# Kernel tuning notes

Measured on AMD Instinct MI355X. Metric: run time of the kernel, lower is better.

## Reference

```python
import jax, jax.numpy as jnp
import numpy as np

EPS = 1e-8  # torch F.cosine_similarity default eps


def setup_inputs() -> dict:
    key = jax.random.key(0)
    k1, k2, k3, k4 = jax.random.split(key, 4)
    B, S, D_in, D_e, E = 4, 128, 768, 256, 100000
    return {
        "x": jax.random.normal(k1, (B, S, D_in), dtype=jnp.float32),
        "W": jax.random.normal(k2, (D_e, D_in), dtype=jnp.float32) * 0.02,
        "b": jax.random.normal(k3, (D_e,), dtype=jnp.float32) * 0.02,
        "entity_embedding": jax.random.normal(k4, (E, D_e), dtype=jnp.float32),
    }


def reference(x, W, b, entity_embedding):
    # Linear projection + tanh: [B,S,D_e]
    q = jnp.tanh(jnp.einsum('bsi,ei->bse', x, W) + b)
    # Cosine similarity = L2-normalize both sides, then GEMM (fused; avoids
    # the [B,S,E,D] broadcast intermediate of the original).
    qn = q / jnp.maximum(jnp.linalg.norm(q, axis=-1, keepdims=True), EPS)
    en = entity_embedding / jnp.maximum(
        jnp.linalg.norm(entity_embedding, axis=-1, keepdims=True), EPS)
    return jnp.einsum('bsd,ed->bse', qn, en)  # [B,S,E]
```

## Files before the change

kernel.cpp:

```cpp
#include <hip/hip_runtime.h>
#include <hip/hip_bf16.h>

#define D_IN  768
#define D_E   256
#define M_TOT 512
#define E_TOT 100000

typedef __attribute__((ext_vector_type(4))) float f32x4;
typedef __attribute__((ext_vector_type(8))) short bf16x8;

__device__ __forceinline__ unsigned short bf16bits(float f) {
    union { __hip_bfloat16 h; unsigned short u; } c;
    c.h = __float2bfloat16(f);
    return c.u;
}

__device__ __forceinline__ void gload_lds16(const void* g, void* l) {
    __builtin_amdgcn_global_load_lds(
        (const __attribute__((address_space(1))) void*)g,
        (__attribute__((address_space(3))) void*)l, 16, 0, 0);
}

#define PROJ_BLOCKS 64
#define PREP_BLOCKS 1563
#define PP_GRID (PROJ_BLOCKS + PREP_BLOCKS)
#define PTM 8
#define PBK 64
#define PROUNDS (D_IN / PBK)

__global__ __launch_bounds__(512) void fused_pp(
    const float* __restrict__ x, const float* __restrict__ W,
    const float* __restrict__ b, const float* __restrict__ en,
    unsigned short* __restrict__ qb, unsigned short* __restrict__ eb)
{
    __shared__ float ws[D_E * (PBK + 1)];
    __shared__ float xs[PTM][PBK];
    __shared__ float red[PTM][4];
    __shared__ float qiv[PTM];

    const int t   = threadIdx.x;
    const int bid = blockIdx.x;

    if (bid >= PROJ_BLOCKS) {
        const int lane = t & 63;
        const int gw   = (bid - PROJ_BLOCKS) * 8 + (t >> 6);
        #pragma unroll 2
        for (int i = 0; i < 8; ++i) {
            const int row = gw * 8 + i;
            if (row >= E_TOT) break;
            const float4 v = *reinterpret_cast<const float4*>(
                en + (size_t)row * D_E + lane * 4);
            float s = v.x*v.x + v.y*v.y + v.z*v.z + v.w*v.w;
            #pragma unroll
            for (int off = 1; off < 64; off <<= 1) s += __shfl_xor(s, off, 64);
            const float sc = 1.0f / fmaxf(sqrtf(s), 1e-8f);
            union { unsigned short u[4]; uint2 d; } o;
            o.u[0] = bf16bits(v.x * sc); o.u[1] = bf16bits(v.y * sc);
            o.u[2] = bf16bits(v.z * sc); o.u[3] = bf16bits(v.w * sc);
            *reinterpret_cast<uint2*>(eb + (size_t)row * D_E + lane * 4) = o.d;
        }
        return;
    }

    const int m0   = bid * PTM;
    const int e    = t & 255;
    const int half = t >> 8;
    const int c4   = t & 15;
    const int rr   = t >> 4;

    float4 wreg[8];
    float  xreg = 0.f;
    float  acc[4] = {0.f, 0.f, 0.f, 0.f};

    #pragma unroll
    for (int i = 0; i < 8; ++i)
        wreg[i] = *reinterpret_cast<const float4*>(
            &W[(size_t)(i * 32 + rr) * D_IN + c4 * 4]);
    xreg = x[(size_t)(m0 + (t >> 6)) * D_IN + (t & 63)];

    for (int rd = 0; rd < PROUNDS; ++rd) {
        #pragma unroll
        for (int i = 0; i < 8; ++i) {
            float* dst = &ws[(i * 32 + rr) * (PBK + 1) + c4 * 4];
            dst[0] = wreg[i].x; dst[1] = wreg[i].y;
            dst[2] = wreg[i].z; dst[3] = wreg[i].w;
        }
        xs[t >> 6][t & 63] = xreg;
        __syncthreads();
        if (rd + 1 < PROUNDS) {
            const int k0 = (rd + 1) * PBK;
            #pragma unroll
            for (int i = 0; i < 8; ++i)
                wreg[i] = *reinterpret_cast<const float4*>(
                    &W[(size_t)(i * 32 + rr) * D_IN + k0 + c4 * 4]);
            xreg = x[(size_t)(m0 + (t >> 6)) * D_IN + k0 + (t & 63)];
        }
        #pragma unroll
        for (int k = 0; k < PBK; ++k) {
            const float wv = ws[e * (PBK + 1) + k];
            #pragma unroll
            for (int j = 0; j < 4; ++j)
                acc[j] = fmaf(xs[half * 4 + j][k], wv, acc[j]);
        }
        __syncthreads();
    }

    const float bias = b[e];
    const int wv4 = (t >> 6) & 3;
    const int lane = t & 63;
    float q[4];
    #pragma unroll
    for (int j = 0; j < 4; ++j) {
        q[j] = tanhf(acc[j] + bias);
        float s = q[j] * q[j];
        #pragma unroll
        for (int off = 1; off < 64; off <<= 1) s += __shfl_xor(s, off, 64);
        if (lane == 0) red[half * 4 + j][wv4] = s;
    }
    __syncthreads();
    if (t < PTM) {
        const float s = red[t][0] + red[t][1] + red[t][2] + red[t][3];
        qiv[t] = 1.0f / fmaxf(sqrtf(s), 1e-8f);
    }
    __syncthreads();
    #pragma unroll
    for (int j = 0; j < 4; ++j)
        qb[(size_t)(m0 + half * 4 + j) * D_E + e] =
            bf16bits(q[j] * qiv[half * 4 + j]);
}

#define BM 128
#define BN 64
#define TPB 25
#define NGRPN 63
#define SIM_GRID (NGRPN * (M_TOT / BM))

__global__ __launch_bounds__(512, 2) void sim_kernel(
    const unsigned short* __restrict__ eb, const unsigned short* __restrict__ qb,
    float* __restrict__ out)
{
    __shared__ unsigned short qs[BM * D_E];
    __shared__ unsigned short es[2][BN * D_E];

    const int t    = threadIdx.x;
    const int lane = t & 63;
    const int wid  = t >> 6;
    const int l15  = lane & 15;
    const int lk   = lane >> 4;
    const int wm   = (wid >> 1) * 32;
    const int wn   = (wid & 1) * 32;

    int vbid;
    {
        const int q = SIM_GRID >> 3, r = SIM_GRID & 7;
        const int xcd = blockIdx.x & 7, rk = blockIdx.x >> 3;
        vbid = (xcd < r ? xcd * (q + 1) : r * (q + 1) + (xcd - r) * q) + rk;
    }
    const int mg    = vbid & 3;
    const int ngrp  = vbid >> 2;
    const int m0    = mg * BM;
    const int nbase = ngrp * (TPB * BN);

    #pragma unroll
    for (int i = 0; i < 8; ++i) {
        const int c   = i * 512 + t;
        const int row = c >> 5;
        const int c16 = c & 31;
        const unsigned short* src =
            qb + (size_t)(m0 + row) * D_E + ((c16 ^ (row & 7)) << 3);
        gload_lds16(src, (void*)&qs[(size_t)c << 3]);
    }
    #pragma unroll
    for (int i = 0; i < 4; ++i) {
        const int c   = i * 512 + t;
        const int row = c >> 5;
        const int c16 = c & 31;
        int rg = nbase + row; if (rg >= E_TOT) rg = E_TOT - 1;
        const unsigned short* src =
            eb + (size_t)rg * D_E + ((c16 ^ (row & 7)) << 3);
        gload_lds16(src, (void*)&es[0][(size_t)c << 3]);
    }

    const char* qsb = reinterpret_cast<const char*>(qs);

    for (int tt = 0; tt < TPB; ++tt) {
        const int n0 = nbase + tt * BN;
        if (n0 >= E_TOT) break;
        const int cur = tt & 1;

        if (tt == 0) {
            asm volatile("s_waitcnt vmcnt(0)" ::: "memory");
        } else {
            asm volatile("s_waitcnt vmcnt(4)" ::: "memory");
        }
        __builtin_amdgcn_s_barrier();
        __builtin_amdgcn_sched_barrier(0);

        const int nn0 = n0 + BN;
        if (tt + 1 < TPB && nn0 < E_TOT) {
            #pragma unroll
            for (int i = 0; i < 4; ++i) {
                const int c   = i * 512 + t;
                const int row = c >> 5;
                const int c16 = c & 31;
                int rg = nn0 + row; if (rg >= E_TOT) rg = E_TOT - 1;
                const unsigned short* src =
                    eb + (size_t)rg * D_E + ((c16 ^ (row & 7)) << 3);
                gload_lds16(src, (void*)&es[cur ^ 1][(size_t)c << 3]);
            }
        }

        const char* esb = reinterpret_cast<const char*>(&es[cur][0]);

        f32x4 acc[2][2];
        #pragma unroll
        for (int mf = 0; mf < 2; ++mf)
            #pragma unroll
            for (int nf = 0; nf < 2; ++nf)
                acc[mf][nf] = (f32x4){0.f, 0.f, 0.f, 0.f};

        __builtin_amdgcn_s_setprio(1);
        #pragma unroll
        for (int ks = 0; ks < 8; ++ks) {
            const int kb = ks * 64 + lk * 16;
            bf16x8 ef[2];
            #pragma unroll
            for (int nf = 0; nf < 2; ++nf) {
                const int row = wn + nf * 16 + l15;
                const int cb  = kb ^ ((row & 7) << 4);
                ef[nf] = *reinterpret_cast<const bf16x8*>(esb + row * 512 + cb);
            }
            #pragma unroll
            for (int mf = 0; mf < 2; ++mf) {
                const int rq  = wm + mf * 16 + l15;
                const int cbq = kb ^ ((rq & 7) << 4);
                const bf16x8 qf =
                    *reinterpret_cast<const bf16x8*>(qsb + rq * 512 + cbq);
                acc[mf][0] = __builtin_amdgcn_mfma_f32_16x16x32_bf16(
                    ef[0], qf, acc[mf][0], 0, 0, 0);
                acc[mf][1] = __builtin_amdgcn_mfma_f32_16x16x32_bf16(
                    ef[1], qf, acc[mf][1], 0, 0, 0);
            }
        }
        __builtin_amdgcn_s_setprio(0);

        #pragma unroll
        for (int mf = 0; mf < 2; ++mf) {
            const int m = m0 + wm + mf * 16 + l15;
            #pragma unroll
            for (int nf = 0; nf < 2; ++nf) {
                const int n = n0 + wn + nf * 16 + lk * 4;
                if (n < E_TOT)
                    *reinterpret_cast<f32x4*>(&out[(size_t)m * E_TOT + n]) =
                        acc[mf][nf];
            }
        }
    }
}

extern "C" void kernel_launch(void* const* d_in, const int* in_sizes, int n_in,
                              void* d_out, int out_size, void* d_ws, size_t ws_size,
                              hipStream_t stream) {
    const float* x  = (const float*)d_in[0];
    const float* W  = (const float*)d_in[1];
    const float* b  = (const float*)d_in[2];
    const float* en = (const float*)d_in[3];
    float* out = (float*)d_out;

    unsigned short* qb = (unsigned short*)d_ws;
    unsigned short* eb = (unsigned short*)((char*)d_ws + (size_t)M_TOT * D_E * 2);

    fused_pp<<<PP_GRID, 512, 0, stream>>>(x, W, b, en, qb, eb);
    sim_kernel<<<SIM_GRID, 512, 0, stream>>>(eb, qb, out);
}
```

Measured before the change: 133.5 us.

## Triple-buffer entity tiles and hoist Q fragments into registers

The entity-tile LDS ring grows from two buffers to three, so each tile is prefetched two iterations ahead. The vmcnt waits are recounted to cover the interleaved output stores. The block's Q fragments are now read from LDS once into registers, instead of being reloaded every k-step of every tile. This cuts LDS read traffic and hides more global-load latency. The cost is 32KB more LDS, about 64 more VGPRs per thread, and redundant clamped prefetches at the end of each group.

```diff
diff --git a/kernel.cpp b/kernel.cpp
--- a/kernel.cpp
+++ b/kernel.cpp
@@ -135,12 +135,28 @@
 #define NGRPN 63
 #define SIM_GRID (NGRPN * (M_TOT / BM))
 
+__device__ __forceinline__ void stage_etile(
+    const unsigned short* __restrict__ eb, int n0, unsigned short* dst, int t)
+{
+    #pragma unroll
+    for (int i = 0; i < 4; ++i) {
+        const int c   = i * 512 + t;
+        const int row = c >> 5;
+        const int c16 = c & 31;
+        int rg = n0 + row;
+        if (rg >= E_TOT) rg = E_TOT - 1;
+        const unsigned short* src =
+            eb + (size_t)rg * D_E + ((c16 ^ (row & 7)) << 3);
+        gload_lds16(src, (void*)&dst[(size_t)c << 3]);
+    }
+}
+
 __global__ __launch_bounds__(512, 2) void sim_kernel(
     const unsigned short* __restrict__ eb, const unsigned short* __restrict__ qb,
     float* __restrict__ out)
 {
     __shared__ unsigned short qs[BM * D_E];
-    __shared__ unsigned short es[2][BN * D_E];
+    __shared__ unsigned short es[3][BN * D_E];
 
     const int t    = threadIdx.x;
     const int lane = t & 63;
@@ -170,45 +186,38 @@
             qb + (size_t)(m0 + row) * D_E + ((c16 ^ (row & 7)) << 3);
         gload_lds16(src, (void*)&qs[(size_t)c << 3]);
     }
-    #pragma unroll
-    for (int i = 0; i < 4; ++i) {
-        const int c   = i * 512 + t;
-        const int row = c >> 5;
-        const int c16 = c & 31;
-        int rg = nbase + row; if (rg >= E_TOT) rg = E_TOT - 1;
-        const unsigned short* src =
-            eb + (size_t)rg * D_E + ((c16 ^ (row & 7)) << 3);
-        gload_lds16(src, (void*)&es[0][(size_t)c << 3]);
-    }
+    stage_etile(eb, nbase,      &es[0][0], t);
+    stage_etile(eb, nbase + BN, &es[1][0], t);
+
+    asm volatile("s_waitcnt vmcnt(8)" ::: "memory");
+    __builtin_amdgcn_s_barrier();
+    __builtin_amdgcn_sched_barrier(0);
 
     const char* qsb = reinterpret_cast<const char*>(qs);
-
+    bf16x8 qf[2][8];
+    #pragma unroll
+    for (int mf = 0; mf < 2; ++mf) {
+        const int rq = wm + mf * 16 + l15;
+        #pragma unroll
+        for (int ks = 0; ks < 8; ++ks) {
+            const int cbq = (ks * 64 + lk * 16) ^ ((rq & 7) << 4);
+            qf[mf][ks] = *reinterpret_cast<const bf16x8*>(qsb + rq * 512 + cbq);
+        }
+    }
+
+    int cur = 0;
     for (int tt = 0; tt < TPB; ++tt) {
         const int n0 = nbase + tt * BN;
         if (n0 >= E_TOT) break;
-        const int cur = tt & 1;
-
-        if (tt == 0) {
-            asm volatile("s_waitcnt vmcnt(0)" ::: "memory");
-        } else {
-            asm volatile("s_waitcnt vmcnt(4)" ::: "memory");
-        }
+
+        if (tt == 0)      asm volatile("s_waitcnt vmcnt(4)"  ::: "memory");
+        else if (tt == 1) asm volatile("s_waitcnt vmcnt(8)"  ::: "memory");
+        else              asm volatile("s_waitcnt vmcnt(12)" ::: "memory");
         __builtin_amdgcn_s_barrier();
         __builtin_amdgcn_sched_barrier(0);
 
-        const int nn0 = n0 + BN;
-        if (tt + 1 < TPB && nn0 < E_TOT) {
-            #pragma unroll
-            for (int i = 0; i < 4; ++i) {
-                const int c   = i * 512 + t;
-                const int row = c >> 5;
-                const int c16 = c & 31;
-                int rg = nn0 + row; if (rg >= E_TOT) rg = E_TOT - 1;
-                const unsigned short* src =
-                    eb + (size_t)rg * D_E + ((c16 ^ (row & 7)) << 3);
-                gload_lds16(src, (void*)&es[cur ^ 1][(size_t)c << 3]);
-            }
-        }
+        int nx = cur + 2; if (nx >= 3) nx -= 3;
+        stage_etile(eb, n0 + 2 * BN, &es[nx][0], t);
 
         const char* esb = reinterpret_cast<const char*>(&es[cur][0]);
 
@@ -232,14 +241,10 @@
             }
             #pragma unroll
             for (int mf = 0; mf < 2; ++mf) {
-                const int rq  = wm + mf * 16 + l15;
-                const int cbq = kb ^ ((rq & 7) << 4);
-                const bf16x8 qf =
-                    *reinterpret_cast<const bf16x8*>(qsb + rq * 512 + cbq);
                 acc[mf][0] = __builtin_amdgcn_mfma_f32_16x16x32_bf16(
-                    ef[0], qf, acc[mf][0], 0, 0, 0);
+                    ef[0], qf[mf][ks], acc[mf][0], 0, 0, 0);
                 acc[mf][1] = __builtin_amdgcn_mfma_f32_16x16x32_bf16(
-                    ef[1], qf, acc[mf][1], 0, 0, 0);
+                    ef[1], qf[mf][ks], acc[mf][1], 0, 0, 0);
             }
         }
         __builtin_amdgcn_s_setprio(0);
@@ -255,6 +260,8 @@
                         acc[mf][nf];
             }
         }
+
+        cur = (cur + 1 == 3) ? 0 : cur + 1;
     }
 }
 
```

Result: slower. 138.6 us (+3.8%).

## Defer output stores by two tiles using double accumulator sets

Applied to the files above, without the earlier changes.

Keeps two accumulator sets and stores the results of the previous two tiles together every other iteration, after the next prefetch has been issued. The vmcnt waits change to match the extra outstanding stores, so global writes overlap later MFMA work instead of sitting at the end of each tile. The cost is more accumulator registers, branches on the buffer parity, and full vmcnt(0) drains on even iterations, which may stall on store completion.

```diff
diff --git a/kernel.cpp b/kernel.cpp
--- a/kernel.cpp
+++ b/kernel.cpp
@@ -183,18 +183,37 @@
 
     const char* qsb = reinterpret_cast<const char*>(qs);
 
-    for (int tt = 0; tt < TPB; ++tt) {
+    f32x4 accA[2][2], accB[2][2];
+
+    #define STORE_TILE(ACC, N0T)                                              \
+        do {                                                                  \
+            _Pragma("unroll")                                                 \
+            for (int mf_ = 0; mf_ < 2; ++mf_) {                               \
+                const int m_ = m0 + wm + mf_ * 16 + l15;                      \
+                _Pragma("unroll")                                             \
+                for (int nf_ = 0; nf_ < 2; ++nf_) {                           \
+                    const int n_ = (N0T) + wn + nf_ * 16 + lk * 4;            \
+                    if (n_ < E_TOT)                                           \
+                        *reinterpret_cast<f32x4*>(                            \
+                            &out[(size_t)m_ * E_TOT + n_]) = ACC[mf_][nf_];   \
+                }                                                             \
+            }                                                                 \
+        } while (0)
+
+    int tt;
+    for (tt = 0; tt < TPB; ++tt) {
         const int n0 = nbase + tt * BN;
         if (n0 >= E_TOT) break;
-        const int cur = tt & 1;
-
-        if (tt == 0) {
+
+        if (tt < 2 || (tt & 1) == 0)
             asm volatile("s_waitcnt vmcnt(0)" ::: "memory");
-        } else {
-            asm volatile("s_waitcnt vmcnt(4)" ::: "memory");
-        }
+        else
+            asm volatile("s_waitcnt vmcnt(8)" ::: "memory");
+        __builtin_amdgcn_sched_barrier(0);
         __builtin_amdgcn_s_barrier();
         __builtin_amdgcn_sched_barrier(0);
+
+        const int cur = tt & 1;
 
         const int nn0 = n0 + BN;
         if (tt + 1 < TPB && nn0 < E_TOT) {
@@ -210,14 +229,26 @@
             }
         }
 
+        if (tt >= 2 && (tt & 1) == 0) {
+            STORE_TILE(accA, nbase + (tt - 2) * BN);
+            STORE_TILE(accB, nbase + (tt - 1) * BN);
+        }
+
         const char* esb = reinterpret_cast<const char*>(&es[cur][0]);
 
-        f32x4 acc[2][2];
-        #pragma unroll
-        for (int mf = 0; mf < 2; ++mf)
-            #pragma unroll
-            for (int nf = 0; nf < 2; ++nf)
-                acc[mf][nf] = (f32x4){0.f, 0.f, 0.f, 0.f};
+        if (cur == 0) {
+            #pragma unroll
+            for (int mf = 0; mf < 2; ++mf)
+                #pragma unroll
+                for (int nf = 0; nf < 2; ++nf)
+                    accA[mf][nf] = (f32x4){0.f, 0.f, 0.f, 0.f};
+        } else {
+            #pragma unroll
+            for (int mf = 0; mf < 2; ++mf)
+                #pragma unroll
+                for (int nf = 0; nf < 2; ++nf)
+                    accB[mf][nf] = (f32x4){0.f, 0.f, 0.f, 0.f};
+        }
 
         __builtin_amdgcn_s_setprio(1);
         #pragma unroll
@@ -236,26 +267,32 @@
                 const int cbq = kb ^ ((rq & 7) << 4);
                 const bf16x8 qf =
                     *reinterpret_cast<const bf16x8*>(qsb + rq * 512 + cbq);
-                acc[mf][0] = __builtin_amdgcn_mfma_f32_16x16x32_bf16(
-                    ef[0], qf, acc[mf][0], 0, 0, 0);
-                acc[mf][1] = __builtin_amdgcn_mfma_f32_16x16x32_bf16(
-                    ef[1], qf, acc[mf][1], 0, 0, 0);
+                if (cur == 0) {
+                    accA[mf][0] = __builtin_amdgcn_mfma_f32_16x16x32_bf16(
+                        ef[0], qf, accA[mf][0], 0, 0, 0);
+                    accA[mf][1] = __builtin_amdgcn_mfma_f32_16x16x32_bf16(
+                        ef[1], qf, accA[mf][1], 0, 0, 0);
+                } else {
+                    accB[mf][0] = __builtin_amdgcn_mfma_f32_16x16x32_bf16(
+                        ef[0], qf, accB[mf][0], 0, 0, 0);
+                    accB[mf][1] = __builtin_amdgcn_mfma_f32_16x16x32_bf16(
+                        ef[1], qf, accB[mf][1], 0, 0, 0);
+                }
             }
         }
         __builtin_amdgcn_s_setprio(0);
-
-        #pragma unroll
-        for (int mf = 0; mf < 2; ++mf) {
-            const int m = m0 + wm + mf * 16 + l15;
-            #pragma unroll
-            for (int nf = 0; nf < 2; ++nf) {
-                const int n = n0 + wn + nf * 16 + lk * 4;
-                if (n < E_TOT)
-                    *reinterpret_cast<f32x4*>(&out[(size_t)m * E_TOT + n]) =
-                        acc[mf][nf];
-            }
-        }
-    }
+    }
+
+    const int lc = tt - 1;
+    if (lc >= 0) {
+        if (lc & 1) {
+            STORE_TILE(accA, nbase + (lc - 1) * BN);
+            STORE_TILE(accB, nbase + lc * BN);
+        } else {
+            STORE_TILE(accA, nbase + lc * BN);
+        }
+    }
+    #undef STORE_TILE
 }
 
 extern "C" void kernel_launch(void* const* d_in, const int* in_sizes, int n_in,
```

Result: slower. 150.6 us (+12.8%).

## Hoist Q fragments to registers and stage output tiles through LDS for coalesced stores

Applied to the files above, without the earlier changes.

Q fragments are loaded once into registers before the tile loop. The Q LDS region is then reused as a double-buffered staging area for the output tile. Each tile's accumulators are written to swizzled LDS and stored to global memory in the next iteration as full 64-float coalesced rows per wave, instead of scattered 16-byte stores, which overlaps the output writes with the next tile's MFMA work. This adds register pressure (32 bf16x8 fragments), extra LDS traffic and more vmcnt bookkeeping.

```diff
diff --git a/kernel.cpp b/kernel.cpp
--- a/kernel.cpp
+++ b/kernel.cpp
@@ -139,7 +139,7 @@
     const unsigned short* __restrict__ eb, const unsigned short* __restrict__ qb,
     float* __restrict__ out)
 {
-    __shared__ unsigned short qs[BM * D_E];
+    __shared__ unsigned short poolA[32768];
     __shared__ unsigned short es[2][BN * D_E];
 
     const int t    = threadIdx.x;
@@ -161,14 +161,16 @@
     const int m0    = mg * BM;
     const int nbase = ngrp * (TPB * BN);
 
+    int nt = (E_TOT - nbase + BN - 1) / BN;
+    if (nt > TPB) nt = TPB;
+
     #pragma unroll
     for (int i = 0; i < 8; ++i) {
         const int c   = i * 512 + t;
         const int row = c >> 5;
         const int c16 = c & 31;
-        const unsigned short* src =
-            qb + (size_t)(m0 + row) * D_E + ((c16 ^ (row & 7)) << 3);
-        gload_lds16(src, (void*)&qs[(size_t)c << 3]);
+        gload_lds16(qb + (size_t)(m0 + row) * D_E + ((c16 ^ (row & 7)) << 3),
+                    (void*)&poolA[(size_t)c << 3]);
     }
     #pragma unroll
     for (int i = 0; i < 4; ++i) {
@@ -176,49 +178,85 @@
         const int row = c >> 5;
         const int c16 = c & 31;
         int rg = nbase + row; if (rg >= E_TOT) rg = E_TOT - 1;
-        const unsigned short* src =
-            eb + (size_t)rg * D_E + ((c16 ^ (row & 7)) << 3);
-        gload_lds16(src, (void*)&es[0][(size_t)c << 3]);
-    }
-
-    const char* qsb = reinterpret_cast<const char*>(qs);
-
-    for (int tt = 0; tt < TPB; ++tt) {
-        const int n0 = nbase + tt * BN;
-        if (n0 >= E_TOT) break;
+        gload_lds16(eb + (size_t)rg * D_E + ((c16 ^ (row & 7)) << 3),
+                    (void*)&es[0][(size_t)c << 3]);
+    }
+
+    asm volatile("s_waitcnt vmcnt(4)" ::: "memory");
+    __builtin_amdgcn_sched_barrier(0);
+    __builtin_amdgcn_s_barrier();
+    __builtin_amdgcn_sched_barrier(0);
+
+    const char* qsb = reinterpret_cast<const char*>(poolA);
+    bf16x8 qf[2][8];
+    #pragma unroll
+    for (int mf = 0; mf < 2; ++mf) {
+        const int rq = wm + mf * 16 + l15;
+        #pragma unroll
+        for (int ks = 0; ks < 8; ++ks) {
+            const int cb = (ks * 64 + lk * 16) ^ ((rq & 7) << 4);
+            qf[mf][ks] = *reinterpret_cast<const bf16x8*>(qsb + rq * 512 + cb);
+        }
+    }
+    asm volatile("s_waitcnt lgkmcnt(0)" ::: "memory");
+    __builtin_amdgcn_sched_barrier(0);
+
+    char* tb[2];
+    tb[0] = reinterpret_cast<char*>(poolA);
+    tb[1] = reinterpret_cast<char*>(poolA) + 32768;
+
+    f32x4 acc[2][2];
+
+    for (int tt = 0; tt < nt; ++tt) {
+        const int n0  = nbase + tt * BN;
         const int cur = tt & 1;
 
-        if (tt == 0) {
-            asm volatile("s_waitcnt vmcnt(0)" ::: "memory");
-        } else {
-            asm volatile("s_waitcnt vmcnt(4)" ::: "memory");
-        }
+        if (tt < 2) asm volatile("s_waitcnt vmcnt(0) lgkmcnt(0)" ::: "memory");
+        else        asm volatile("s_waitcnt vmcnt(16) lgkmcnt(0)" ::: "memory");
+        __builtin_amdgcn_sched_barrier(0);
         __builtin_amdgcn_s_barrier();
         __builtin_amdgcn_sched_barrier(0);
 
-        const int nn0 = n0 + BN;
-        if (tt + 1 < TPB && nn0 < E_TOT) {
+        if (tt + 1 < nt) {
+            const int nn0 = n0 + BN;
             #pragma unroll
             for (int i = 0; i < 4; ++i) {
                 const int c   = i * 512 + t;
                 const int row = c >> 5;
                 const int c16 = c & 31;
                 int rg = nn0 + row; if (rg >= E_TOT) rg = E_TOT - 1;
-                const unsigned short* src =
-                    eb + (size_t)rg * D_E + ((c16 ^ (row & 7)) << 3);
-                gload_lds16(src, (void*)&es[cur ^ 1][(size_t)c << 3]);
-            }
-        }
-
-        const char* esb = reinterpret_cast<const char*>(&es[cur][0]);
-
-        f32x4 acc[2][2];
+                gload_lds16(eb + (size_t)rg * D_E + ((c16 ^ (row & 7)) << 3),
+                            (void*)&es[cur ^ 1][(size_t)c << 3]);
+            }
+        }
+
+        if (tt >= 1) {
+            const char* tbp = tb[cur ^ 1];
+            const int  n0p  = n0 - BN;
+            float v[16];
+            #pragma unroll
+            for (int j = 0; j < 16; ++j) {
+                const int row = wid * 16 + j;
+                v[j] = *reinterpret_cast<const float*>(
+                    tbp + row * 256 + ((lane * 4) ^ ((row & 7) << 4)));
+            }
+            const int n = n0p + lane;
+            if (n < E_TOT) {
+                #pragma unroll
+                for (int j = 0; j < 16; ++j) {
+                    const int row = wid * 16 + j;
+                    out[(size_t)(m0 + row) * E_TOT + n] = v[j];
+                }
+            }
+        }
+
         #pragma unroll
         for (int mf = 0; mf < 2; ++mf)
             #pragma unroll
             for (int nf = 0; nf < 2; ++nf)
                 acc[mf][nf] = (f32x4){0.f, 0.f, 0.f, 0.f};
 
+        const char* esb = reinterpret_cast<const char*>(&es[cur][0]);
         __builtin_amdgcn_s_setprio(1);
         #pragma unroll
         for (int ks = 0; ks < 8; ++ks) {
@@ -232,27 +270,50 @@
             }
             #pragma unroll
             for (int mf = 0; mf < 2; ++mf) {
-                const int rq  = wm + mf * 16 + l15;
-                const int cbq = kb ^ ((rq & 7) << 4);
-                const bf16x8 qf =
-                    *reinterpret_cast<const bf16x8*>(qsb + rq * 512 + cbq);
                 acc[mf][0] = __builtin_amdgcn_mfma_f32_16x16x32_bf16(
-                    ef[0], qf, acc[mf][0], 0, 0, 0);
+                    ef[0], qf[mf][ks], acc[mf][0], 0, 0, 0);
                 acc[mf][1] = __builtin_amdgcn_mfma_f32_16x16x32_bf16(
-                    ef[1], qf, acc[mf][1], 0, 0, 0);
+                    ef[1], qf[mf][ks], acc[mf][1], 0, 0, 0);
             }
         }
         __builtin_amdgcn_s_setprio(0);
 
-        #pragma unroll
-        for (int mf = 0; mf < 2; ++mf) {
-            const int m = m0 + wm + mf * 16 + l15;
-            #pragma unroll
-            for (int nf = 0; nf < 2; ++nf) {
-                const int n = n0 + wn + nf * 16 + lk * 4;
-                if (n < E_TOT)
-                    *reinterpret_cast<f32x4*>(&out[(size_t)m * E_TOT + n]) =
+        {
+            char* tbp = tb[cur];
+            #pragma unroll
+            for (int mf = 0; mf < 2; ++mf) {
+                const int mrow = wm + mf * 16 + l15;
+                #pragma unroll
+                for (int nf = 0; nf < 2; ++nf) {
+                    const int colb = (wn + nf * 16 + lk * 4) * 4;
+                    *reinterpret_cast<f32x4*>(
+                        tbp + mrow * 256 + (colb ^ ((mrow & 7) << 4))) =
                         acc[mf][nf];
+                }
+            }
+        }
+    }
+
+    asm volatile("s_waitcnt lgkmcnt(0)" ::: "memory");
+    __builtin_amdgcn_sched_barrier(0);
+    __builtin_amdgcn_s_barrier();
+    __builtin_amdgcn_sched_barrier(0);
+    {
+        const char* tbp = tb[(nt - 1) & 1];
+        const int  n0p  = nbase + (nt - 1) * BN;
+        float v[16];
+        #pragma unroll
+        for (int j = 0; j < 16; ++j) {
+            const int row = wid * 16 + j;
+            v[j] = *reinterpret_cast<const float*>(
+                tbp + row * 256 + ((lane * 4) ^ ((row & 7) << 4)));
+        }
+        const int n = n0p + lane;
+        if (n < E_TOT) {
+            #pragma unroll
+            for (int j = 0; j < 16; ++j) {
+                const int row = wid * 16 + j;
+                out[(size_t)(m0 + row) * E_TOT + n] = v[j];
             }
         }
     }
```

Result: slower. 141.5 us (+6.0%).
